# Kernel tuning notes

Hardware: AMD Instinct MI355X
Metric: run time of the kernel (lower is better)

Reference implementation:

```python
import jax, jax.numpy as jnp
import numpy as np

HIDDEN = 512
HEADS = 8
HEAD_DIM = HIDDEN // HEADS
BATCH = 4096
SEQ = 16


def setup_inputs() -> dict:
    key = jax.random.key(0)
    k1, k2, k3 = jax.random.split(key, 3)
    scale = 1.0 / np.sqrt(HIDDEN)
    return {
        "hidden_states": jax.random.normal(k1, (BATCH, SEQ, HIDDEN), dtype=jnp.float32),
        # torch Linear(hidden, 3*hidden, bias=False): weight shape [3*hidden, hidden]
        "w_qkv": jax.random.uniform(k2, (3 * HIDDEN, HIDDEN), dtype=jnp.float32, minval=-scale, maxval=scale),
        "w_o": jax.random.uniform(k3, (HIDDEN, HIDDEN), dtype=jnp.float32, minval=-scale, maxval=scale),
    }


def reference(hidden_states, w_qkv, w_o):
    b, s, _ = hidden_states.shape
    # fused QKV projection: y = x @ W^T
    qkv = jnp.einsum("bsh,oh->bso", hidden_states, w_qkv)
    qkv = qkv.reshape(b, s, 3, HEADS, HEAD_DIM)
    qkv = jnp.transpose(qkv, (2, 0, 3, 1, 4))  # [3, b, heads, s, head_dim]
    q, k, v = qkv[0], qkv[1], qkv[2]
    # scaled dot-product attention (non-causal, dropout=0 in eval)
    scores = jnp.einsum("bhqd,bhkd->bhqk", q, k) / jnp.sqrt(jnp.float32(HEAD_DIM))
    probs = jax.nn.softmax(scores, axis=-1)
    attn = jnp.einsum("bhqk,bhkd->bhqd", probs, v)
    attn = jnp.transpose(attn, (0, 2, 1, 3)).reshape(b, s, HIDDEN)
    return jnp.einsum("bsh,oh->bso", attn, w_o)
```

## Files before the change

### kernel.cpp

```cpp
#include <hip/hip_runtime.h>


#define HID 512

typedef __attribute__((ext_vector_type(4))) float  float4v;
typedef __attribute__((ext_vector_type(8))) short  short8;
typedef __attribute__((ext_vector_type(4))) short  short4v;
typedef __attribute__((ext_vector_type(8))) __bf16 bf16x8;

static __device__ __forceinline__ short bf16rne(float f) {
    union { float f; unsigned u; } v; v.f = f;
    unsigned u = v.u + 0x7FFFu + ((v.u >> 16) & 1u);
    return (short)(u >> 16);
}

static __device__ __forceinline__ short8 pack8(float4v a, float4v b) {
    short8 o;
    o[0] = bf16rne(a[0]); o[1] = bf16rne(a[1]); o[2] = bf16rne(a[2]); o[3] = bf16rne(a[3]);
    o[4] = bf16rne(b[0]); o[5] = bf16rne(b[1]); o[6] = bf16rne(b[2]); o[7] = bf16rne(b[3]);
    return o;
}

static __device__ __forceinline__ void cvt8_store(short* dst, const float* src) {
    float4v a = *(const float4v*)src;
    float4v b = *(const float4v*)(src + 4);
    *(short8*)dst = pack8(a, b);
}

static __device__ __forceinline__ float4v mfma16(short8 a, short8 b, float4v c) {
    union { short8 s; bf16x8 v; } ua, ub;
    ua.s = a; ub.s = b;
    return __builtin_amdgcn_mfma_f32_16x16x32_bf16(ua.v, ub.v, c, 0, 0, 0);
}

static __device__ __forceinline__ void gld16(const short* g, short* l) {
    __builtin_amdgcn_global_load_lds(
        (const __attribute__((address_space(1))) void*)g,
        (__attribute__((address_space(3))) void*)l,
        16, 0, 0);
}

__global__ void cvt_kernel(const float* __restrict__ src, short* __restrict__ dst, int n4) {
    int i = blockIdx.x * 256 + threadIdx.x;
    if (i >= n4) return;
    float4v v = *(const float4v*)(src + (size_t)i * 4);
    short4v o;
    o[0] = bf16rne(v[0]); o[1] = bf16rne(v[1]); o[2] = bf16rne(v[2]); o[3] = bf16rne(v[3]);
    *(short4v*)(dst + (size_t)i * 4) = o;
}

__global__ __launch_bounds__(512, 4)
void qkv_head_kernel(const float* __restrict__ x, const short* __restrict__ xb, const int use_xb,
                     const float* __restrict__ wqf, const short* __restrict__ wqb, const int use_wb,
                     short* __restrict__ attnb, float* __restrict__ attnf, const int use_ab) {
    __shared__ __align__(16) union {
        struct { short a[2][128 * 64]; short b[2][192 * 64]; } st;
        struct { short q[128 * 72]; short k[128 * 72]; short vt[64 * 152]; short p[8 * 16 * 40]; } at;
    } L;

    const int tid  = threadIdx.x;
    const int wave = tid >> 6;
    const int lane = tid & 63;
    const int ln   = lane & 15;
    const int q8   = (lane >> 4) * 8;
    const int qrow = (lane >> 4) * 4;
    const int wr   = wave >> 2;
    const int wc   = wave & 3;

    const int g   = blockIdx.x;
    const int xcd = g & 7;
    const int j   = g >> 3;
    const int h   = j & 7;
    const int mt  = (j >> 3) * 8 + xcd;
    const int m0  = mt * 128;

    float4v acc[4][3];
    #pragma unroll
    for (int fr = 0; fr < 4; ++fr)
        #pragma unroll
        for (int fc = 0; fc < 3; ++fc)
            acc[fr][fc] = (float4v){0.f, 0.f, 0.f, 0.f};

    auto stageA = [&](int buf, int kb) {
        if (use_xb) {
            #pragma unroll
            for (int i = 0; i < 2; ++i) {
                const int cg  = i * 512 + tid;
                const int row = cg >> 3;
                const int c8  = ((cg & 7) ^ (row & 7)) * 8;
                gld16(&xb[(size_t)(m0 + row) * HID + kb * 64 + c8],
                      &L.st.a[buf][(i * 512 + (wave << 6)) * 8]);
            }
        } else {
            #pragma unroll
            for (int i = 0; i < 2; ++i) {
                const int cg  = i * 512 + tid;
                const int row = cg >> 3;
                const int c8  = ((cg & 7) ^ (row & 7)) * 8;
                cvt8_store(&L.st.a[buf][cg * 8], &x[(size_t)(m0 + row) * HID + kb * 64 + c8]);
            }
        }
    };
    auto stageB = [&](int buf, int kb) {
        if (use_wb) {
            #pragma unroll
            for (int i = 0; i < 3; ++i) {
                const int cg   = i * 512 + tid;
                const int n    = cg >> 3;
                const int c8   = ((cg & 7) ^ (n & 7)) * 8;
                const int grow = (n >> 6) * HID + h * 64 + (n & 63);
                gld16(&wqb[(size_t)grow * HID + kb * 64 + c8],
                      &L.st.b[buf][(i * 512 + (wave << 6)) * 8]);
            }
        } else {
            #pragma unroll
            for (int i = 0; i < 3; ++i) {
                const int cg   = i * 512 + tid;
                const int n    = cg >> 3;
                const int c8   = ((cg & 7) ^ (n & 7)) * 8;
                const int grow = (n >> 6) * HID + h * 64 + (n & 63);
                cvt8_store(&L.st.b[buf][cg * 8], &wqf[(size_t)grow * HID + kb * 64 + c8]);
            }
        }
    };

    stageA(0, 0);
    stageB(0, 0);
    __syncthreads();

    int cur = 0;
    for (int kb = 0; kb < 8; ++kb) {
        if (kb < 7) {
            stageA(cur ^ 1, kb + 1);
            stageB(cur ^ 1, kb + 1);
        }
        #pragma unroll
        for (int ks = 0; ks < 2; ++ks) {
            const int cslot = ks * 4 + (lane >> 4);
            short8 a[4], b[3];
            #pragma unroll
            for (int fr = 0; fr < 4; ++fr) {
                const int row = wr * 64 + fr * 16 + ln;
                a[fr] = *(const short8*)&L.st.a[cur][row * 64 + ((cslot ^ (row & 7)) << 3)];
            }
            #pragma unroll
            for (int fc = 0; fc < 3; ++fc) {
                const int row = wc * 48 + fc * 16 + ln;
                b[fc] = *(const short8*)&L.st.b[cur][row * 64 + ((cslot ^ (row & 7)) << 3)];
            }
            #pragma unroll
            for (int fr = 0; fr < 4; ++fr)
                #pragma unroll
                for (int fc = 0; fc < 3; ++fc)
                    acc[fr][fc] = mfma16(a[fr], b[fc], acc[fr][fc]);
        }
        __syncthreads();
        cur ^= 1;
    }

    #pragma unroll
    for (int fr = 0; fr < 4; ++fr) {
        #pragma unroll
        for (int fc = 0; fc < 3; ++fc) {
            const int nb = wc * 48 + fc * 16;
            const int n  = nb + ln;
            const int mb = wr * 64 + fr * 16 + qrow;
            const float4v v = acc[fr][fc];
            if (nb < 64) {
                #pragma unroll
                for (int r = 0; r < 4; ++r)
                    L.at.q[(mb + r) * 72 + n] = bf16rne(v[r] * 0.125f);
            } else if (nb < 128) {
                #pragma unroll
                for (int r = 0; r < 4; ++r)
                    L.at.k[(mb + r) * 72 + (n - 64)] = bf16rne(v[r]);
            } else {
                #pragma unroll
                for (int r = 0; r < 4; ++r)
                    L.at.vt[(n - 128) * 152 + mb + r] = bf16rne(v[r]);
            }
        }
    }
    for (int i = tid; i < 64 * 24; i += 512)
        L.at.vt[(i / 24) * 152 + 128 + (i % 24)] = 0;
    for (int i = tid; i < 8 * 16 * 16; i += 512)
        L.at.p[(i >> 8) * 640 + ((i >> 4) & 15) * 40 + 16 + (i & 15)] = 0;
    __syncthreads();

    {
        const int rb = wave * 16;
        const short* qp = &L.at.q[(rb + ln) * 72 + q8];
        const short* kp = &L.at.k[(rb + ln) * 72 + q8];
        short8 aq0 = *(const short8*)qp;
        short8 aq1 = *(const short8*)(qp + 32);
        short8 bk0 = *(const short8*)kp;
        short8 bk1 = *(const short8*)(kp + 32);
        float4v s = (float4v){0.f, 0.f, 0.f, 0.f};
        s = mfma16(aq0, bk0, s);
        s = mfma16(aq1, bk1, s);

        float4v mx = s;
        #pragma unroll
        for (int off = 1; off < 16; off <<= 1)
            #pragma unroll
            for (int r = 0; r < 4; ++r)
                mx[r] = fmaxf(mx[r], __shfl_xor(mx[r], off));
        float4v p;
        #pragma unroll
        for (int r = 0; r < 4; ++r) p[r] = __expf(s[r] - mx[r]);
        float4v sm = p;
        #pragma unroll
        for (int off = 1; off < 16; off <<= 1)
            #pragma unroll
            for (int r = 0; r < 4; ++r)
                sm[r] += __shfl_xor(sm[r], off);
        #pragma unroll
        for (int r = 0; r < 4; ++r)
            L.at.p[wave * 640 + (qrow + r) * 40 + ln] = bf16rne(p[r] * __builtin_amdgcn_rcpf(sm[r]));

        short8 ap = *(const short8*)&L.at.p[wave * 640 + ln * 40 + q8];
        #pragma unroll
        for (int dc = 0; dc < 4; ++dc) {
            short8 bv = *(const short8*)&L.at.vt[(dc * 16 + ln) * 152 + rb + q8];
            float4v o = (float4v){0.f, 0.f, 0.f, 0.f};
            o = mfma16(ap, bv, o);
            #pragma unroll
            for (int r = 0; r < 4; ++r) {
                const size_t oi = (size_t)(m0 + rb + qrow + r) * HID + h * 64 + dc * 16 + ln;
                if (use_ab) attnb[oi] = bf16rne(o[r]);
                else        attnf[oi] = o[r];
            }
        }
    }
}

__global__ __launch_bounds__(512, 4)
void oproj_kernel(const short* __restrict__ attnb,
                  const float* __restrict__ wof, const short* __restrict__ wob,
                  const int use_wb, float* __restrict__ out) {
    __shared__ __align__(16) short A[2][128 * 64];
    __shared__ __align__(16) short B[2][128 * 64];

    const int tid  = threadIdx.x;
    const int wave = tid >> 6;
    const int lane = tid & 63;
    const int ln   = lane & 15;
    const int q8   = (lane >> 4) * 8;
    const int qrow = (lane >> 4) * 4;
    const int wr   = wave >> 2;
    const int wc   = wave & 3;

    const int g   = blockIdx.x;
    const int xcd = g & 7;
    const int j   = g >> 3;
    const int nt  = j & 3;
    const int mt  = (j >> 2) * 8 + xcd;
    const int m0  = mt * 128;
    const int n0  = nt * 128;

    float4v acc[4][2];
    #pragma unroll
    for (int fr = 0; fr < 4; ++fr)
        #pragma unroll
        for (int fc = 0; fc < 2; ++fc)
            acc[fr][fc] = (float4v){0.f, 0.f, 0.f, 0.f};

    auto stage = [&](int buf, int kb) {
        #pragma unroll
        for (int i = 0; i < 2; ++i) {
            const int cg  = i * 512 + tid;
            const int row = cg >> 3;
            const int c8  = ((cg & 7) ^ (row & 7)) * 8;
            gld16(&attnb[(size_t)(m0 + row) * HID + kb * 64 + c8],
                  &A[buf][(i * 512 + (wave << 6)) * 8]);
            if (use_wb)
                gld16(&wob[(size_t)(n0 + row) * HID + kb * 64 + c8],
                      &B[buf][(i * 512 + (wave << 6)) * 8]);
            else
                cvt8_store(&B[buf][cg * 8], &wof[(size_t)(n0 + row) * HID + kb * 64 + c8]);
        }
    };

    stage(0, 0);
    __syncthreads();

    int cur = 0;
    for (int kb = 0; kb < 8; ++kb) {
        if (kb < 7) stage(cur ^ 1, kb + 1);
        #pragma unroll
        for (int ks = 0; ks < 2; ++ks) {
            const int cslot = ks * 4 + (lane >> 4);
            short8 a[4], b[2];
            #pragma unroll
            for (int fr = 0; fr < 4; ++fr) {
                const int row = wr * 64 + fr * 16 + ln;
                a[fr] = *(const short8*)&A[cur][row * 64 + ((cslot ^ (row & 7)) << 3)];
            }
            #pragma unroll
            for (int fc = 0; fc < 2; ++fc) {
                const int row = wc * 32 + fc * 16 + ln;
                b[fc] = *(const short8*)&B[cur][row * 64 + ((cslot ^ (row & 7)) << 3)];
            }
            #pragma unroll
            for (int fr = 0; fr < 4; ++fr)
                #pragma unroll
                for (int fc = 0; fc < 2; ++fc)
                    acc[fr][fc] = mfma16(a[fr], b[fc], acc[fr][fc]);
        }
        __syncthreads();
        cur ^= 1;
    }

    #pragma unroll
    for (int fr = 0; fr < 4; ++fr)
        #pragma unroll
        for (int fc = 0; fc < 2; ++fc)
            #pragma unroll
            for (int r = 0; r < 4; ++r)
                out[(size_t)(m0 + wr * 64 + fr * 16 + qrow + r) * HID +
                    n0 + wc * 32 + fc * 16 + ln] = acc[fr][fc][r];
}

__global__ __launch_bounds__(512, 2)
void oproj_inplace_kernel(float* __restrict__ io, const float* __restrict__ wof,
                          const short* __restrict__ wob, const int use_wb) {
    __shared__ __align__(16) short sA[64 * 40];
    __shared__ __align__(16) short sW2[512 * 40];

    const int tid  = threadIdx.x;
    const int wave = tid >> 6;
    const int lane = tid & 63;
    const int ln   = lane & 15;
    const int q8   = (lane >> 4) * 8;
    const int qrow = (lane >> 4) * 4;
    const int m0   = blockIdx.x * 64;

    float4v acc[4][4];
    #pragma unroll
    for (int fr = 0; fr < 4; ++fr)
        #pragma unroll
        for (int fc = 0; fc < 4; ++fc)
            acc[fr][fc] = (float4v){0.f, 0.f, 0.f, 0.f};

    for (int kb = 0; kb < 16; ++kb) {
        __syncthreads();
        if (tid < 256) {
            int row = tid >> 2, c8 = (tid & 3) * 8;
            cvt8_store(&sA[row * 40 + c8], &io[(size_t)(m0 + row) * HID + kb * 32 + c8]);
        }
        #pragma unroll
        for (int it = 0; it < 4; ++it) {
            int gg = tid + it * 512;
            int n = gg >> 2, c8 = (gg & 3) * 8;
            if (use_wb)
                *(short8*)&sW2[n * 40 + c8] = *(const short8*)&wob[(size_t)n * HID + kb * 32 + c8];
            else
                cvt8_store(&sW2[n * 40 + c8], &wof[(size_t)n * HID + kb * 32 + c8]);
        }
        __syncthreads();
        short8 a[4], b[4];
        #pragma unroll
        for (int fr = 0; fr < 4; ++fr)
            a[fr] = *(const short8*)&sA[(fr * 16 + ln) * 40 + q8];
        #pragma unroll
        for (int fc = 0; fc < 4; ++fc)
            b[fc] = *(const short8*)&sW2[(wave * 64 + fc * 16 + ln) * 40 + q8];
        #pragma unroll
        for (int fr = 0; fr < 4; ++fr)
            #pragma unroll
            for (int fc = 0; fc < 4; ++fc)
                acc[fr][fc] = mfma16(a[fr], b[fc], acc[fr][fc]);
    }
    #pragma unroll
    for (int fr = 0; fr < 4; ++fr)
        #pragma unroll
        for (int fc = 0; fc < 4; ++fc)
            #pragma unroll
            for (int r = 0; r < 4; ++r)
                io[(size_t)(m0 + fr * 16 + qrow + r) * HID + wave * 64 + fc * 16 + ln] =
                    acc[fr][fc][r];
}

extern "C" void kernel_launch(void* const* d_in, const int* in_sizes, int n_in,
                              void* d_out, int out_size, void* d_ws, size_t ws_size,
                              hipStream_t stream) {
    const float* x    = (const float*)d_in[0];
    const float* wqkv = (const float*)d_in[1];
    const float* wo   = (const float*)d_in[2];
    float* out = (float*)d_out;

    const size_t n_x  = (size_t)65536 * HID;
    const size_t n_wq = (size_t)1536 * HID;
    const size_t n_wo = (size_t)HID * HID;
    const size_t szA = (n_x * 2 + n_wq + n_wo) * 2;
    const size_t szB = (n_x + n_wq + n_wo) * 2;
    const size_t szC = (n_wq + n_wo) * 2;

    short* xb = nullptr; short* attnb = nullptr; short* wqb = nullptr; short* wob = nullptr;
    int use_xb = 0, use_ab = 0, use_wb = 0;
    short* ws = (short*)d_ws;

    if (d_ws && ws_size >= szA) {
        use_xb = use_ab = use_wb = 1;
        xb = ws; attnb = xb + n_x; wqb = attnb + n_x; wob = wqb + n_wq;
    } else if (d_ws && ws_size >= szB) {
        use_ab = use_wb = 1;
        attnb = ws; wqb = attnb + n_x; wob = wqb + n_wq;
    } else if (d_ws && ws_size >= szC) {
        use_wb = 1;
        wqb = ws; wob = wqb + n_wq;
    }

    if (use_xb)
        cvt_kernel<<<(int)(n_x / 1024), 256, 0, stream>>>(x, xb, (int)(n_x / 4));
    if (use_wb) {
        cvt_kernel<<<(int)(n_wq / 1024), 256, 0, stream>>>(wqkv, wqb, (int)(n_wq / 4));
        cvt_kernel<<<(int)(n_wo / 1024), 256, 0, stream>>>(wo, wob, (int)(n_wo / 4));
    }

    qkv_head_kernel<<<4096, 512, 0, stream>>>(x, xb, use_xb, wqkv, wqb, use_wb,
                                              attnb, out , use_ab);

    if (use_ab)
        oproj_kernel<<<2048, 512, 0, stream>>>(attnb, wo, wob, use_wb, out);
    else
        oproj_inplace_kernel<<<1024, 512, 0, stream>>>(out, wo, wob, use_wb);
}
```

Baseline: 379.4 us.

## Pre-pack weights into MFMA fragment order and load B directly to registers

Weight matrices are repacked once into per-lane MFMA fragment order, so the QKV and output-projection GEMMs load B operands straight from global (L2-resident) into registers with a triple-buffered prefetch, dropping the LDS staging and the LDS reads for B. The output-projection kernel also moves to 256-thread blocks with a 4x4 fragment tile per wave. This cuts LDS footprint and traffic, which may raise occupancy, at the cost of more registers and per-wave global weight loads.

```diff
diff --git a/kernel.cpp b/kernel.cpp
--- a/kernel.cpp
+++ b/kernel.cpp
@@ -49,12 +49,35 @@
     *(short4v*)(dst + (size_t)i * 4) = o;
 }
 
+__global__ void repack_wq_kernel(const float* __restrict__ src, short* __restrict__ dst) {
+    int i = blockIdx.x * 256 + threadIdx.x;
+    int lane = i & 63, t = i >> 6;
+    int g = t % 12; t /= 12;
+    int ks = t & 1; t >>= 1;
+    int kb = t & 7; int h = t >> 3;
+    int n = g * 16 + (lane & 15);
+    int grow = (n >> 6) * HID + h * 64 + (n & 63);
+    int col = kb * 64 + ks * 32 + (lane >> 4) * 8;
+    cvt8_store(&dst[(size_t)i * 8], &src[(size_t)grow * HID + col]);
+}
+
+__global__ void repack_wo_kernel(const float* __restrict__ src, short* __restrict__ dst) {
+    int i = blockIdx.x * 256 + threadIdx.x;
+    int lane = i & 63, t = i >> 6;
+    int gg = t & 7; t >>= 3;
+    int ks = t & 1; t >>= 1;
+    int kb = t & 7; int nt = t >> 3;
+    int row = nt * 128 + gg * 16 + (lane & 15);
+    int col = kb * 64 + ks * 32 + (lane >> 4) * 8;
+    cvt8_store(&dst[(size_t)i * 8], &src[(size_t)row * HID + col]);
+}
+
 __global__ __launch_bounds__(512, 4)
 void qkv_head_kernel(const float* __restrict__ x, const short* __restrict__ xb, const int use_xb,
                      const float* __restrict__ wqf, const short* __restrict__ wqb, const int use_wb,
                      short* __restrict__ attnb, float* __restrict__ attnf, const int use_ab) {
     __shared__ __align__(16) union {
-        struct { short a[2][128 * 64]; short b[2][192 * 64]; } st;
+        struct { short a[2][128 * 64]; } st;
         struct { short q[128 * 72]; short k[128 * 72]; short vt[64 * 152]; short p[8 * 16 * 40]; } at;
     } L;
 
@@ -101,61 +124,68 @@
             }
         }
     };
-    auto stageB = [&](int buf, int kb) {
+    auto loadKs = [&](short8* d, int kb, int ks) {
         if (use_wb) {
             #pragma unroll
-            for (int i = 0; i < 3; ++i) {
-                const int cg   = i * 512 + tid;
-                const int n    = cg >> 3;
-                const int c8   = ((cg & 7) ^ (n & 7)) * 8;
+            for (int fc = 0; fc < 3; ++fc) {
+                const int chunk = ((h * 8 + kb) * 2 + ks) * 12 + wc * 3 + fc;
+                d[fc] = *(const short8*)&wqb[(size_t)chunk * 512 + lane * 8];
+            }
+        } else {
+            #pragma unroll
+            for (int fc = 0; fc < 3; ++fc) {
+                const int n    = (wc * 3 + fc) * 16 + ln;
                 const int grow = (n >> 6) * HID + h * 64 + (n & 63);
-                gld16(&wqb[(size_t)grow * HID + kb * 64 + c8],
-                      &L.st.b[buf][(i * 512 + (wave << 6)) * 8]);
-            }
-        } else {
-            #pragma unroll
-            for (int i = 0; i < 3; ++i) {
-                const int cg   = i * 512 + tid;
-                const int n    = cg >> 3;
-                const int c8   = ((cg & 7) ^ (n & 7)) * 8;
-                const int grow = (n >> 6) * HID + h * 64 + (n & 63);
-                cvt8_store(&L.st.b[buf][cg * 8], &wqf[(size_t)grow * HID + kb * 64 + c8]);
+                const float* s = &wqf[(size_t)grow * HID + kb * 64 + ks * 32 + q8];
+                d[fc] = pack8(*(const float4v*)s, *(const float4v*)(s + 4));
             }
         }
     };
 
+    short8 bf[3][3];
+    loadKs(bf[0], 0, 0);
+    loadKs(bf[1], 0, 1);
     stageA(0, 0);
-    stageB(0, 0);
     __syncthreads();
 
-    int cur = 0;
+    #pragma unroll
     for (int kb = 0; kb < 8; ++kb) {
+        const int cur = kb & 1;
+        const int s0 = (2 * kb) % 3, s1 = (2 * kb + 1) % 3, sf = (2 * kb + 2) % 3;
         if (kb < 7) {
             stageA(cur ^ 1, kb + 1);
-            stageB(cur ^ 1, kb + 1);
-        }
-        #pragma unroll
-        for (int ks = 0; ks < 2; ++ks) {
-            const int cslot = ks * 4 + (lane >> 4);
-            short8 a[4], b[3];
+            loadKs(bf[sf], kb + 1, 0);
+        }
+        {
+            const int cslot = (lane >> 4);
+            short8 a[4];
             #pragma unroll
             for (int fr = 0; fr < 4; ++fr) {
                 const int row = wr * 64 + fr * 16 + ln;
                 a[fr] = *(const short8*)&L.st.a[cur][row * 64 + ((cslot ^ (row & 7)) << 3)];
             }
             #pragma unroll
-            for (int fc = 0; fc < 3; ++fc) {
-                const int row = wc * 48 + fc * 16 + ln;
-                b[fc] = *(const short8*)&L.st.b[cur][row * 64 + ((cslot ^ (row & 7)) << 3)];
-            }
-            #pragma unroll
             for (int fr = 0; fr < 4; ++fr)
                 #pragma unroll
                 for (int fc = 0; fc < 3; ++fc)
-                    acc[fr][fc] = mfma16(a[fr], b[fc], acc[fr][fc]);
+                    acc[fr][fc] = mfma16(a[fr], bf[s0][fc], acc[fr][fc]);
+        }
+        if (kb < 7) loadKs(bf[s0], kb + 1, 1);
+        {
+            const int cslot = 4 + (lane >> 4);
+            short8 a[4];
+            #pragma unroll
+            for (int fr = 0; fr < 4; ++fr) {
+                const int row = wr * 64 + fr * 16 + ln;
+                a[fr] = *(const short8*)&L.st.a[cur][row * 64 + ((cslot ^ (row & 7)) << 3)];
+            }
+            #pragma unroll
+            for (int fr = 0; fr < 4; ++fr)
+                #pragma unroll
+                for (int fc = 0; fc < 3; ++fc)
+                    acc[fr][fc] = mfma16(a[fr], bf[s1][fc], acc[fr][fc]);
         }
         __syncthreads();
-        cur ^= 1;
     }
 
     #pragma unroll
@@ -234,21 +264,18 @@
     }
 }
 
-__global__ __launch_bounds__(512, 4)
-void oproj_kernel(const short* __restrict__ attnb,
-                  const float* __restrict__ wof, const short* __restrict__ wob,
-                  const int use_wb, float* __restrict__ out) {
+__global__ __launch_bounds__(256, 3)
+void oproj_kernel(const short* __restrict__ attnb, const short* __restrict__ wob,
+                  float* __restrict__ out) {
     __shared__ __align__(16) short A[2][128 * 64];
-    __shared__ __align__(16) short B[2][128 * 64];
 
     const int tid  = threadIdx.x;
     const int wave = tid >> 6;
     const int lane = tid & 63;
     const int ln   = lane & 15;
-    const int q8   = (lane >> 4) * 8;
     const int qrow = (lane >> 4) * 4;
-    const int wr   = wave >> 2;
-    const int wc   = wave & 3;
+    const int wr   = wave >> 1;
+    const int wc   = wave & 1;
 
     const int g   = blockIdx.x;
     const int xcd = g & 7;
@@ -258,67 +285,85 @@
     const int m0  = mt * 128;
     const int n0  = nt * 128;
 
-    float4v acc[4][2];
+    float4v acc[4][4];
     #pragma unroll
     for (int fr = 0; fr < 4; ++fr)
         #pragma unroll
-        for (int fc = 0; fc < 2; ++fc)
+        for (int fc = 0; fc < 4; ++fc)
             acc[fr][fc] = (float4v){0.f, 0.f, 0.f, 0.f};
 
-    auto stage = [&](int buf, int kb) {
-        #pragma unroll
-        for (int i = 0; i < 2; ++i) {
-            const int cg  = i * 512 + tid;
+    auto stageA = [&](int buf, int kb) {
+        #pragma unroll
+        for (int i = 0; i < 4; ++i) {
+            const int cg  = i * 256 + tid;
             const int row = cg >> 3;
             const int c8  = ((cg & 7) ^ (row & 7)) * 8;
             gld16(&attnb[(size_t)(m0 + row) * HID + kb * 64 + c8],
-                  &A[buf][(i * 512 + (wave << 6)) * 8]);
-            if (use_wb)
-                gld16(&wob[(size_t)(n0 + row) * HID + kb * 64 + c8],
-                      &B[buf][(i * 512 + (wave << 6)) * 8]);
-            else
-                cvt8_store(&B[buf][cg * 8], &wof[(size_t)(n0 + row) * HID + kb * 64 + c8]);
+                  &A[buf][(i * 256 + (wave << 6)) * 8]);
         }
     };
-
-    stage(0, 0);
+    auto loadKs = [&](short8* d, int kb, int ks) {
+        #pragma unroll
+        for (int fc = 0; fc < 4; ++fc) {
+            const int chunk = ((nt * 8 + kb) * 2 + ks) * 8 + wc * 4 + fc;
+            d[fc] = *(const short8*)&wob[(size_t)chunk * 512 + lane * 8];
+        }
+    };
+
+    short8 bf[3][4];
+    loadKs(bf[0], 0, 0);
+    loadKs(bf[1], 0, 1);
+    stageA(0, 0);
     __syncthreads();
 
-    int cur = 0;
+    #pragma unroll
     for (int kb = 0; kb < 8; ++kb) {
-        if (kb < 7) stage(cur ^ 1, kb + 1);
-        #pragma unroll
-        for (int ks = 0; ks < 2; ++ks) {
-            const int cslot = ks * 4 + (lane >> 4);
-            short8 a[4], b[2];
+        const int cur = kb & 1;
+        const int s0 = (2 * kb) % 3, s1 = (2 * kb + 1) % 3, sf = (2 * kb + 2) % 3;
+        if (kb < 7) {
+            stageA(cur ^ 1, kb + 1);
+            loadKs(bf[sf], kb + 1, 0);
+        }
+        {
+            const int cslot = (lane >> 4);
+            short8 a[4];
             #pragma unroll
             for (int fr = 0; fr < 4; ++fr) {
                 const int row = wr * 64 + fr * 16 + ln;
                 a[fr] = *(const short8*)&A[cur][row * 64 + ((cslot ^ (row & 7)) << 3)];
             }
             #pragma unroll
-            for (int fc = 0; fc < 2; ++fc) {
-                const int row = wc * 32 + fc * 16 + ln;
-                b[fc] = *(const short8*)&B[cur][row * 64 + ((cslot ^ (row & 7)) << 3)];
-            }
-            #pragma unroll
             for (int fr = 0; fr < 4; ++fr)
                 #pragma unroll
-                for (int fc = 0; fc < 2; ++fc)
-                    acc[fr][fc] = mfma16(a[fr], b[fc], acc[fr][fc]);
+                for (int fc = 0; fc < 4; ++fc)
+                    acc[fr][fc] = mfma16(a[fr], bf[s0][fc], acc[fr][fc]);
+        }
+        if (kb < 7) loadKs(bf[s0], kb + 1, 1);
+        {
+            const int cslot = 4 + (lane >> 4);
+            short8 a[4];
+            #pragma unroll
+            for (int fr = 0; fr < 4; ++fr) {
+                const int row = wr * 64 + fr * 16 + ln;
+                a[fr] = *(const short8*)&A[cur][row * 64 + ((cslot ^ (row & 7)) << 3)];
+            }
+            #pragma unroll
+            for (int fr = 0; fr < 4; ++fr)
+                #pragma unroll
+                for (int fc = 0; fc < 4; ++fc)
+                    acc[fr][fc] = mfma16(a[fr], bf[s1][fc], acc[fr][fc]);
         }
         __syncthreads();
-        cur ^= 1;
     }
 
     #pragma unroll
     for (int fr = 0; fr < 4; ++fr)
         #pragma unroll
-        for (int fc = 0; fc < 2; ++fc)
+        for (int fc = 0; fc < 4; ++fc)
             #pragma unroll
             for (int r = 0; r < 4; ++r)
                 out[(size_t)(m0 + wr * 64 + fr * 16 + qrow + r) * HID +
-                    n0 + wc * 32 + fc * 16 + ln] = acc[fr][fc][r];
+                    n0 + wc * 64 + fc * 16 + ln] = acc[fr][fc][r];
 }
 
 __global__ __launch_bounds__(512, 2)
@@ -414,15 +459,18 @@
     if (use_xb)
         cvt_kernel<<<(int)(n_x / 1024), 256, 0, stream>>>(x, xb, (int)(n_x / 4));
     if (use_wb) {
-        cvt_kernel<<<(int)(n_wq / 1024), 256, 0, stream>>>(wqkv, wqb, (int)(n_wq / 4));
-        cvt_kernel<<<(int)(n_wo / 1024), 256, 0, stream>>>(wo, wob, (int)(n_wo / 4));
+        repack_wq_kernel<<<384, 256, 0, stream>>>(wqkv, wqb);
+        if (use_ab)
+            repack_wo_kernel<<<128, 256, 0, stream>>>(wo, wob);
+        else
+            cvt_kernel<<<(int)(n_wo / 1024), 256, 0, stream>>>(wo, wob, (int)(n_wo / 4));
     }
 
     qkv_head_kernel<<<4096, 512, 0, stream>>>(x, xb, use_xb, wqkv, wqb, use_wb,
                                               attnb, out , use_ab);
 
     if (use_ab)
-        oproj_kernel<<<2048, 512, 0, stream>>>(attnb, wo, wob, use_wb, out);
+        oproj_kernel<<<2048, 256, 0, stream>>>(attnb, wob, out);
     else
         oproj_inplace_kernel<<<1024, 512, 0, stream>>>(out, wo, wob, use_wb);
 }
```

Measured after the change: 408.9 us. 7.8% more time.
